# Kernel optimization log

Hardware: AMD Instinct MI355X
Metric: run time of the kernel (lower is better)

## Reference

```python
import jax, jax.numpy as jnp
import numpy as np

B, T, D, W, H = 8, 2048, 1024, 16, 8
HD = D // H  # head dim = 128
EPS = 1e-5


def _layernorm(x, g, b):
    m = jnp.mean(x, axis=-1, keepdims=True)
    v = jnp.var(x, axis=-1, keepdims=True)
    return (x - m) / jnp.sqrt(v + EPS) * g + b


def setup_inputs() -> dict:
    key = jax.random.key(0)
    ks = jax.random.split(key, 8)
    s = 0.02
    return {
        "frame_features": jax.random.normal(ks[0], (B, T, D), dtype=jnp.float32),
        "frame_indices": jnp.arange(B * T, dtype=jnp.int64).reshape(B, T),
        # nn.MultiheadAttention packed in-projection (3D, D) and out projection
        "w_qkv": jax.random.normal(ks[1], (3 * D, D), dtype=jnp.float32) * s,
        "b_qkv": jnp.zeros((3 * D,), dtype=jnp.float32),
        "w_out": jax.random.normal(ks[2], (D, D), dtype=jnp.float32) * s,
        "b_out": jnp.zeros((D,), dtype=jnp.float32),
        # FFN: Linear(D, 4D) -> GELU -> Linear(4D, D)
        "w1": jax.random.normal(ks[3], (4 * D, D), dtype=jnp.float32) * s,
        "b1": jnp.zeros((4 * D,), dtype=jnp.float32),
        "w2": jax.random.normal(ks[4], (D, 4 * D), dtype=jnp.float32) * s,
        "b2": jnp.zeros((D,), dtype=jnp.float32),
        "g1": jnp.ones((D,), dtype=jnp.float32),
        "beta1": jnp.zeros((D,), dtype=jnp.float32),
        "g2": jnp.ones((D,), dtype=jnp.float32),
        "beta2": jnp.zeros((D,), dtype=jnp.float32),
    }


def _forward(frame_features, frame_indices, w_qkv, b_qkv, w_out, b_out,
             w1, b1, w2, b2, g1, beta1, g2, beta2):
    # --- sinusoidal temporal positional encoding, indexed by frame number ---
    pos = frame_indices.astype(jnp.float32)[..., None]          # (B, T, 1)
    div = jnp.exp(-jnp.log(10000.0) * jnp.arange(0, D, 2, dtype=jnp.float32) / D)
    ang = pos * div                                              # (B, T, D/2)
    pe = jnp.stack([jnp.sin(ang), jnp.cos(ang)], axis=-1).reshape(B, T, D)
    x = frame_features + pe

    # --- block-diagonal (local window) attention, all windows in one pass ---
    nw = T // W
    xw = x.reshape(B, nw, W, D)
    qkv = jnp.einsum('bnwd,ed->bnwe', xw, w_qkv) + b_qkv         # (B, nw, W, 3D)
    q, k, v = jnp.split(qkv, 3, axis=-1)
    q = q.reshape(B, nw, W, H, HD)
    k = k.reshape(B, nw, W, H, HD)
    v = v.reshape(B, nw, W, H, HD)
    scores = jnp.einsum('bnqhd,bnkhd->bnhqk', q, k) / jnp.sqrt(jnp.float32(HD))
    attn = jax.nn.softmax(scores, axis=-1)
    o = jnp.einsum('bnhqk,bnkhd->bnqhd', attn, v).reshape(B, nw, W, D)
    attn_out = jnp.einsum('bnwd,ed->bnwe', o, w_out) + b_out

    h = _layernorm(xw + attn_out, g1, beta1)
    ffn = jnp.einsum('bnwf,df->bnwd', jax.nn.gelu(
        jnp.einsum('bnwd,fd->bnwf', h, w1) + b1, approximate=False), w2) + b2
    out = _layernorm(h + ffn, g2, beta2)
    return out.reshape(B, T, D)


def reference(frame_features, frame_indices, w_qkv, b_qkv, w_out, b_out,
              w1, b1, w2, b2, g1, beta1, g2, beta2):
    return _forward(frame_features, frame_indices, w_qkv, b_qkv, w_out, b_out,
                    w1, b1, w2, b2, g1, beta1, g2, beta2)
```

## Files before the change

kernel.cpp:

```cpp
#include <hip/hip_runtime.h>
#include <math.h>

typedef __bf16 bf16;
typedef __bf16 bf16x8 __attribute__((ext_vector_type(8)));
typedef __bf16 bf16x4 __attribute__((ext_vector_type(4)));
typedef __bf16 bf16x2 __attribute__((ext_vector_type(2)));
typedef float f32x4 __attribute__((ext_vector_type(4)));

#define ROWS 16384

typedef __attribute__((address_space(3))) void* lds_vp;
typedef const __attribute__((address_space(1))) void* glb_vp;
__device__ __forceinline__ void gload16(const void* g, void* l) {
  __builtin_amdgcn_global_load_lds((glb_vp)g, (lds_vp)l, 16, 0, 0);
}

__global__ __launch_bounds__(256) void cast_kernel(
    const float* __restrict__ src, bf16* __restrict__ dst, int n)
{
  int i = (blockIdx.x * 256 + threadIdx.x) * 8;
  if (i >= n) return;
  float4 a = *(const float4*)(src + i);
  float4 b = *(const float4*)(src + i + 4);
  bf16x8 o;
  o[0] = (bf16)a.x; o[1] = (bf16)a.y; o[2] = (bf16)a.z; o[3] = (bf16)a.w;
  o[4] = (bf16)b.x; o[5] = (bf16)b.y; o[6] = (bf16)b.z; o[7] = (bf16)b.w;
  *(bf16x8*)(dst + i) = o;
}

__global__ __launch_bounds__(256) void pe_add_kernel(
    const float* __restrict__ ff, const int* __restrict__ idx, bf16* __restrict__ x)
{
  int p   = blockIdx.x * 256 + threadIdx.x;
  int row = p >> 9;
  int j   = p & 511;
  float pos = (float)idx[row];
  float d2  = (float)(2 * j) * (1.0f / 1024.0f);
  float dv  = expf(-9.210340371976184f * d2);
  float ang = pos * dv;
  float s, c;
  sincosf(ang, &s, &c);
  int base = row * 1024 + 2 * j;
  float2 f = *(const float2*)(ff + base);
  bf16x2 o;
  o[0] = (bf16)(f.x + s);
  o[1] = (bf16)(f.y + c);
  *(bf16x2*)(x + base) = o;
}

#define MFMA16 __builtin_amdgcn_mfma_f32_16x16x32_bf16
#define SB  __builtin_amdgcn_sched_barrier(0)
#define BAR asm volatile("s_barrier" ::: "memory")

template<bool GELU, bool RES>
__global__ __launch_bounds__(512, 2) void gemm8(
    const bf16* __restrict__ A, const bf16* __restrict__ Bw,
    const float* __restrict__ bias, const bf16* __restrict__ resid,
    bf16* __restrict__ C, int M, int N, int K)
{
  extern __shared__ char smem[];
  bf16* lA = (bf16*)smem;
  bf16* lB = (bf16*)(smem + 65536);

  const int tid  = threadIdx.x;
  const int wave = tid >> 6;
  const int lane = tid & 63;
  const int wm = wave >> 2, wn = wave & 3;
  const int ln = lane & 15, q = lane >> 4;
  const int wm8 = wm * 8, wn4 = wn * 4;
  const int rsw = (ln * 32 + q * 8) ^ (((ln >> 3) & 1) << 4);

  const int nwg = gridDim.x;
  const int nbm = M >> 8;
  const int swz = (blockIdx.x & 7) * (nwg >> 3) + (blockIdx.x >> 3);
  const int bm = (swz % nbm) << 8;
  const int bn = (swz / nbm) << 8;

  const int le = lane ^ (((lane >> 5) & 1) << 1);
  const int sr = le >> 2;
  const int sc = (le & 3) * 8;
  const bf16* gA = A  + (size_t)(bm + wave * 16 + sr) * K + sc;
  const bf16* gB = Bw + (size_t)(bn + wave * 16 + sr) * K + sc;
  const size_t hstep = (size_t)128 * K;

#define STAGE_A(h, bb, kk) do { \
    bf16* _d = lA + (bb) * 16384 + ((h) * 8 + wave) * 1024; \
    gload16(gA + (size_t)(h) * hstep + (kk), _d); \
    gload16(gA + (size_t)(h) * hstep + (kk) + 32, _d + 512); } while (0)
#define STAGE_B(h, bb, kk) do { \
    bf16* _d = lB + (bb) * 16384 + ((h) * 8 + wave) * 1024; \
    gload16(gB + (size_t)(h) * hstep + (kk), _d); \
    gload16(gB + (size_t)(h) * hstep + (kk) + 32, _d + 512); } while (0)
#define LDA8(dst, t, ks, bb) (dst) = *(const bf16x8*)(lA + (bb) * 16384 + (wm8 + (t)) * 1024 + (ks) * 512 + rsw)
#define LDB8(dst, n, ks, bb) (dst) = *(const bf16x8*)(lB + (bb) * 16384 + (wn4 + (n)) * 1024 + (ks) * 512 + rsw)

  f32x4 acc[8][4];
#pragma unroll
  for (int i = 0; i < 8; i++)
#pragma unroll
    for (int j = 0; j < 4; j++) acc[i][j] = {0.f, 0.f, 0.f, 0.f};

  const int nkt = K >> 6;

  STAGE_A(0, 0, 0);  STAGE_A(1, 0, 0);
  STAGE_B(0, 0, 0);  STAGE_B(1, 0, 0);
  STAGE_A(0, 1, 64); STAGE_A(1, 1, 64);
  SB; asm volatile("s_waitcnt vmcnt(4)" ::: "memory"); SB;
  BAR; SB;

  bf16x8 alo[4][2], ahi[4][2], bq[2][2];

  for (int m = 0; m < nkt; ++m) {
    const int b  = m & 1;
    const int k0 = m << 6;

#pragma unroll
    for (int t = 0; t < 4; t++) { LDA8(alo[t][0], t, 0, b); LDA8(alo[t][1], t, 1, b); }
    LDB8(bq[0][0], 0, 0, b); LDB8(bq[0][1], 0, 1, b);
    LDB8(bq[1][0], 1, 0, b); LDB8(bq[1][1], 1, 1, b);
    if (m + 1 < nkt) STAGE_B(0, b ^ 1, k0 + 64);
    SB; BAR; SB;
    __builtin_amdgcn_s_setprio(1);
#pragma unroll
    for (int t = 0; t < 4; t++)
#pragma unroll
      for (int n = 0; n < 2; n++) {
        acc[t][n] = MFMA16(alo[t][0], bq[n][0], acc[t][n], 0, 0, 0);
        acc[t][n] = MFMA16(alo[t][1], bq[n][1], acc[t][n], 0, 0, 0);
      }
    __builtin_amdgcn_s_setprio(0);
    SB; BAR; SB;

#pragma unroll
    for (int t = 0; t < 4; t++) { LDA8(ahi[t][0], t + 4, 0, b); LDA8(ahi[t][1], t + 4, 1, b); }
    if (m + 1 < nkt) STAGE_B(1, b ^ 1, k0 + 64);
    SB; BAR; SB;
    __builtin_amdgcn_s_setprio(1);
#pragma unroll
    for (int t = 0; t < 4; t++)
#pragma unroll
      for (int n = 0; n < 2; n++) {
        acc[t + 4][n] = MFMA16(ahi[t][0], bq[n][0], acc[t + 4][n], 0, 0, 0);
        acc[t + 4][n] = MFMA16(ahi[t][1], bq[n][1], acc[t + 4][n], 0, 0, 0);
      }
    __builtin_amdgcn_s_setprio(0);
    SB; BAR; SB;

    LDB8(bq[0][0], 2, 0, b); LDB8(bq[0][1], 2, 1, b);
    LDB8(bq[1][0], 3, 0, b); LDB8(bq[1][1], 3, 1, b);
    if (m + 2 < nkt) STAGE_A(0, b, k0 + 128);
    SB; BAR; SB;
    __builtin_amdgcn_s_setprio(1);
#pragma unroll
    for (int t = 0; t < 4; t++)
#pragma unroll
      for (int n = 0; n < 2; n++) {
        acc[t][n + 2] = MFMA16(alo[t][0], bq[n][0], acc[t][n + 2], 0, 0, 0);
        acc[t][n + 2] = MFMA16(alo[t][1], bq[n][1], acc[t][n + 2], 0, 0, 0);
      }
    __builtin_amdgcn_s_setprio(0);
    SB; BAR; SB;

    if (m + 2 < nkt) STAGE_A(1, b, k0 + 128);
    SB; BAR; SB;
    __builtin_amdgcn_s_setprio(1);
#pragma unroll
    for (int t = 0; t < 4; t++)
#pragma unroll
      for (int n = 0; n < 2; n++) {
        acc[t + 4][n + 2] = MFMA16(ahi[t][0], bq[n][0], acc[t + 4][n + 2], 0, 0, 0);
        acc[t + 4][n + 2] = MFMA16(ahi[t][1], bq[n][1], acc[t + 4][n + 2], 0, 0, 0);
      }
    __builtin_amdgcn_s_setprio(0);
    SB;
    if (m == nkt - 2)     { asm volatile("s_waitcnt vmcnt(0)" ::: "memory"); }
    else if (m < nkt - 2) { asm volatile("s_waitcnt vmcnt(4)" ::: "memory"); }
    SB; BAR; SB;
  }

  float bv[4];
#pragma unroll
  for (int tn = 0; tn < 4; tn++) bv[tn] = bias[bn + wn * 64 + tn * 16 + ln];
  bf16* eb = (bf16*)smem;
  const int lrow = tid >> 4;
  const int cb   = (tid & 15) * 16;
#pragma unroll
  for (int tm = 0; tm < 8; tm++) {
    __syncthreads();
#pragma unroll
    for (int tn = 0; tn < 4; tn++)
#pragma unroll
      for (int i = 0; i < 4; i++)
        eb[(wm * 16 + q * 4 + i) * 264 + wn * 64 + tn * 16 + ln] =
            (bf16)(acc[tm][tn][i] + bv[tn]);
    __syncthreads();
    int gR = bm + (lrow >> 4) * 128 + tm * 16 + (lrow & 15);
    size_t rowoff = (size_t)gR * N + bn + cb;
    bf16x8 v0 = *(const bf16x8*)&eb[lrow * 264 + cb];
    bf16x8 v1 = *(const bf16x8*)&eb[lrow * 264 + cb + 8];
    if (RES) {
      bf16x8 r0 = *(const bf16x8*)(resid + rowoff);
      bf16x8 r1 = *(const bf16x8*)(resid + rowoff + 8);
#pragma unroll
      for (int u = 0; u < 8; u++) {
        v0[u] = (bf16)((float)v0[u] + (float)r0[u]);
        v1[u] = (bf16)((float)v1[u] + (float)r1[u]);
      }
    }
    if (GELU) {
#pragma unroll
      for (int u = 0; u < 8; u++) {
        float a = (float)v0[u], c = (float)v1[u];
        v0[u] = (bf16)(0.5f * a * (1.0f + erff(a * 0.70710678118654752f)));
        v1[u] = (bf16)(0.5f * c * (1.0f + erff(c * 0.70710678118654752f)));
      }
    }
    *(bf16x8*)(C + rowoff)     = v0;
    *(bf16x8*)(C + rowoff + 8) = v1;
  }
#undef STAGE_A
#undef STAGE_B
#undef LDA8
#undef LDB8
}

__global__ __launch_bounds__(256) void attn_kernel(
    const bf16* __restrict__ qkv, bf16* __restrict__ o)
{
  __shared__ float sq[16][132], sk[16][132], sv[16][132];
  __shared__ float ss[16][17];

  int wid = blockIdx.x;
  int h   = wid & 7;
  int win = wid >> 3;
  int tb  = win * 16;

  int t  = threadIdx.x;
  int r  = t >> 4;
  int c8 = (t & 15) * 8;

  const bf16* base = qkv + (size_t)(tb + r) * 3072 + c8;
  bf16x8 qv = *(const bf16x8*)(base + h * 128);
  bf16x8 kv = *(const bf16x8*)(base + 1024 + h * 128);
  bf16x8 vv = *(const bf16x8*)(base + 2048 + h * 128);
#pragma unroll
  for (int u = 0; u < 8; u++) {
    sq[r][c8 + u] = (float)qv[u];
    sk[r][c8 + u] = (float)kv[u];
    sv[r][c8 + u] = (float)vv[u];
  }
  __syncthreads();

  {
    int i = t >> 4, jj = t & 15;
    float s = 0.f;
#pragma unroll 8
    for (int d = 0; d < 128; d++) s += sq[i][d] * sk[jj][d];
    ss[i][jj] = s * 0.08838834764831845f;
  }
  __syncthreads();

  if (t < 16) {
    float m = -1e30f;
    for (int jj = 0; jj < 16; jj++) m = fmaxf(m, ss[t][jj]);
    float sum = 0.f;
    for (int jj = 0; jj < 16; jj++) { float e = expf(ss[t][jj] - m); ss[t][jj] = e; sum += e; }
    float inv = 1.0f / sum;
    for (int jj = 0; jj < 16; jj++) ss[t][jj] *= inv;
  }
  __syncthreads();

  {
    int i = t >> 4; int d0 = (t & 15) * 8;
    float acc[8] = {0, 0, 0, 0, 0, 0, 0, 0};
#pragma unroll
    for (int jj = 0; jj < 16; jj++) {
      float a = ss[i][jj];
#pragma unroll
      for (int u = 0; u < 8; u++) acc[u] += a * sv[jj][d0 + u];
    }
    bf16* op = o + (size_t)(tb + i) * 1024 + h * 128 + d0;
#pragma unroll
    for (int u = 0; u < 8; u++) op[u] = (bf16)acc[u];
  }
}

template<typename OUT_T>
__global__ __launch_bounds__(256) void ln_kernel(
    const bf16* __restrict__ x, const float* __restrict__ g,
    const float* __restrict__ b, OUT_T* __restrict__ y)
{
  __shared__ float red[8];
  int row = blockIdx.x;
  int t   = threadIdx.x;
  int lane = t & 63, wave = t >> 6;

  bf16x4 v4 = *(const bf16x4*)(x + (size_t)row * 1024 + t * 4);
  float v[4];
  float s = 0.f, sq = 0.f;
#pragma unroll
  for (int u = 0; u < 4; u++) {
    v[u] = (float)v4[u];
    s += v[u];
    sq += v[u] * v[u];
  }
  for (int off = 32; off > 0; off >>= 1) {
    s  += __shfl_down(s, off);
    sq += __shfl_down(sq, off);
  }
  if (lane == 0) { red[wave * 2] = s; red[wave * 2 + 1] = sq; }
  __syncthreads();
  float st = red[0] + red[2] + red[4] + red[6];
  float qt = red[1] + red[3] + red[5] + red[7];
  float mean = st * (1.0f / 1024.0f);
  float var  = qt * (1.0f / 1024.0f) - mean * mean;
  float inv  = rsqrtf(var + 1e-5f);
  int c = t * 4;
  OUT_T* yr = y + (size_t)row * 1024 + c;
#pragma unroll
  for (int u = 0; u < 4; u++)
    yr[u] = (OUT_T)((v[u] - mean) * inv * g[c + u] + b[c + u]);
}

extern "C" void kernel_launch(void* const* d_in, const int* in_sizes, int n_in,
                              void* d_out, int out_size, void* d_ws, size_t ws_size,
                              hipStream_t stream) {
  const float* ff    = (const float*)d_in[0];
  const int*   idx   = (const int*)d_in[1];
  const float* w_qkv = (const float*)d_in[2];
  const float* b_qkv = (const float*)d_in[3];
  const float* w_out = (const float*)d_in[4];
  const float* b_out = (const float*)d_in[5];
  const float* w1    = (const float*)d_in[6];
  const float* b1    = (const float*)d_in[7];
  const float* w2    = (const float*)d_in[8];
  const float* b2    = (const float*)d_in[9];
  const float* g1    = (const float*)d_in[10];
  const float* be1   = (const float*)d_in[11];
  const float* g2    = (const float*)d_in[12];
  const float* be2   = (const float*)d_in[13];
  float* out = (float*)d_out;

  static bool attrs_done = false;
  if (!attrs_done) {
    attrs_done = true;
    hipFuncSetAttribute(reinterpret_cast<const void*>(&gemm8<false, false>),
                        hipFuncAttributeMaxDynamicSharedMemorySize, 131072);
    hipFuncSetAttribute(reinterpret_cast<const void*>(&gemm8<false, true>),
                        hipFuncAttributeMaxDynamicSharedMemorySize, 131072);
    hipFuncSetAttribute(reinterpret_cast<const void*>(&gemm8<true, false>),
                        hipFuncAttributeMaxDynamicSharedMemorySize, 131072);
  }

  char* p = (char*)d_ws;
  bf16* x_bf = (bf16*)p;  p += (size_t)ROWS * 1024 * 2;
  bf16* big  = (bf16*)p;  p += (size_t)ROWS * 4096 * 2;
  bf16* s_bf = (bf16*)p;  p += (size_t)ROWS * 1024 * 2;
  bf16* h_bf = (bf16*)p;  p += (size_t)ROWS * 1024 * 2;
  bf16* wqb  = (bf16*)p;  p += (size_t)3072 * 1024 * 2;
  bf16* wob  = (bf16*)p;  p += (size_t)1024 * 1024 * 2;
  bf16* w1b  = (bf16*)p;  p += (size_t)4096 * 1024 * 2;
  bf16* w2b  = (bf16*)p;  p += (size_t)1024 * 4096 * 2;
  bf16* o_bf = big + (size_t)ROWS * 3072;
  bf16* g_bf = big;

  cast_kernel<<<3072 * 1024 / 8 / 256, 256, 0, stream>>>(w_qkv, wqb, 3072 * 1024);
  cast_kernel<<<1024 * 1024 / 8 / 256, 256, 0, stream>>>(w_out, wob, 1024 * 1024);
  cast_kernel<<<4096 * 1024 / 8 / 256, 256, 0, stream>>>(w1, w1b, 4096 * 1024);
  cast_kernel<<<1024 * 4096 / 8 / 256, 256, 0, stream>>>(w2, w2b, 1024 * 4096);

  pe_add_kernel<<<ROWS * 512 / 256, 256, 0, stream>>>(ff, idx, x_bf);

  gemm8<false, false><<<64 * 12, 512, 131072, stream>>>(
      x_bf, wqb, b_qkv, nullptr, big, ROWS, 3072, 1024);
  attn_kernel<<<(ROWS / 16) * 8, 256, 0, stream>>>(big, o_bf);
  gemm8<false, true><<<64 * 4, 512, 131072, stream>>>(
      o_bf, wob, b_out, x_bf, s_bf, ROWS, 1024, 1024);
  ln_kernel<bf16><<<ROWS, 256, 0, stream>>>(s_bf, g1, be1, h_bf);
  gemm8<true, false><<<64 * 16, 512, 131072, stream>>>(
      h_bf, w1b, b1, nullptr, big, ROWS, 4096, 1024);
  gemm8<false, true><<<64 * 4, 512, 131072, stream>>>(
      g_bf, w2b, b2, h_bf, s_bf, ROWS, 1024, 4096);
  ln_kernel<float><<<ROWS, 256, 0, stream>>>(s_bf, g2, be2, out);
}
```

Before: 727.2 us.

## Reorder GEMM tile mapping, relax barrier memory clobbers, use tanh-approx GELU

Changes the workgroup-to-tile mapping so consecutive swizzled blocks walk along N instead of M. Replaces inline-asm barriers that had memory clobbers with the builtin s_barrier and adds explicit lgkmcnt waits, giving the compiler more freedom to schedule. Replaces the erf-based GELU in the epilogue with a tanh approximation built from exp2 and rcp. This makes GELU cheaper but departs from the exact erf GELU the reference specifies.

```diff
diff --git a/kernel.cpp b/kernel.cpp
--- a/kernel.cpp
+++ b/kernel.cpp
@@ -50,7 +50,6 @@
 
 #define MFMA16 __builtin_amdgcn_mfma_f32_16x16x32_bf16
 #define SB  __builtin_amdgcn_sched_barrier(0)
-#define BAR asm volatile("s_barrier" ::: "memory")
 
 template<bool GELU, bool RES>
 __global__ __launch_bounds__(512, 2) void gemm8(
@@ -71,10 +70,10 @@
   const int rsw = (ln * 32 + q * 8) ^ (((ln >> 3) & 1) << 4);
 
   const int nwg = gridDim.x;
-  const int nbm = M >> 8;
+  const int nbn = N >> 8;
   const int swz = (blockIdx.x & 7) * (nwg >> 3) + (blockIdx.x >> 3);
-  const int bm = (swz % nbm) << 8;
-  const int bn = (swz / nbm) << 8;
+  const int bm = (swz / nbn) << 8;
+  const int bn = (swz % nbn) << 8;
 
   const int le = lane ^ (((lane >> 5) & 1) << 1);
   const int sr = le >> 2;
@@ -105,8 +104,8 @@
   STAGE_A(0, 0, 0);  STAGE_A(1, 0, 0);
   STAGE_B(0, 0, 0);  STAGE_B(1, 0, 0);
   STAGE_A(0, 1, 64); STAGE_A(1, 1, 64);
-  SB; asm volatile("s_waitcnt vmcnt(4)" ::: "memory"); SB;
-  BAR; SB;
+  SB; asm volatile("s_waitcnt vmcnt(4)"); SB;
+  __builtin_amdgcn_s_barrier();
 
   bf16x8 alo[4][2], ahi[4][2], bq[2][2];
 
@@ -119,7 +118,9 @@
     LDB8(bq[0][0], 0, 0, b); LDB8(bq[0][1], 0, 1, b);
     LDB8(bq[1][0], 1, 0, b); LDB8(bq[1][1], 1, 1, b);
     if (m + 1 < nkt) STAGE_B(0, b ^ 1, k0 + 64);
-    SB; BAR; SB;
+    __builtin_amdgcn_s_barrier();
+    asm volatile("s_waitcnt lgkmcnt(0)");
+    SB;
     __builtin_amdgcn_s_setprio(1);
 #pragma unroll
     for (int t = 0; t < 4; t++)
@@ -129,12 +130,14 @@
         acc[t][n] = MFMA16(alo[t][1], bq[n][1], acc[t][n], 0, 0, 0);
       }
     __builtin_amdgcn_s_setprio(0);
-    SB; BAR; SB;
+    __builtin_amdgcn_s_barrier();
 
 #pragma unroll
     for (int t = 0; t < 4; t++) { LDA8(ahi[t][0], t + 4, 0, b); LDA8(ahi[t][1], t + 4, 1, b); }
     if (m + 1 < nkt) STAGE_B(1, b ^ 1, k0 + 64);
-    SB; BAR; SB;
+    __builtin_amdgcn_s_barrier();
+    asm volatile("s_waitcnt lgkmcnt(0)");
+    SB;
     __builtin_amdgcn_s_setprio(1);
 #pragma unroll
     for (int t = 0; t < 4; t++)
@@ -144,12 +147,14 @@
         acc[t + 4][n] = MFMA16(ahi[t][1], bq[n][1], acc[t + 4][n], 0, 0, 0);
       }
     __builtin_amdgcn_s_setprio(0);
-    SB; BAR; SB;
+    __builtin_amdgcn_s_barrier();
 
     LDB8(bq[0][0], 2, 0, b); LDB8(bq[0][1], 2, 1, b);
     LDB8(bq[1][0], 3, 0, b); LDB8(bq[1][1], 3, 1, b);
     if (m + 2 < nkt) STAGE_A(0, b, k0 + 128);
-    SB; BAR; SB;
+    __builtin_amdgcn_s_barrier();
+    asm volatile("s_waitcnt lgkmcnt(0)");
+    SB;
     __builtin_amdgcn_s_setprio(1);
 #pragma unroll
     for (int t = 0; t < 4; t++)
@@ -159,10 +164,10 @@
         acc[t][n + 2] = MFMA16(alo[t][1], bq[n][1], acc[t][n + 2], 0, 0, 0);
       }
     __builtin_amdgcn_s_setprio(0);
-    SB; BAR; SB;
+    __builtin_amdgcn_s_barrier();
 
     if (m + 2 < nkt) STAGE_A(1, b, k0 + 128);
-    SB; BAR; SB;
+    __builtin_amdgcn_s_barrier();
     __builtin_amdgcn_s_setprio(1);
 #pragma unroll
     for (int t = 0; t < 4; t++)
@@ -173,9 +178,10 @@
       }
     __builtin_amdgcn_s_setprio(0);
     SB;
-    if (m == nkt - 2)     { asm volatile("s_waitcnt vmcnt(0)" ::: "memory"); }
-    else if (m < nkt - 2) { asm volatile("s_waitcnt vmcnt(4)" ::: "memory"); }
-    SB; BAR; SB;
+    if (m == nkt - 2)     { asm volatile("s_waitcnt vmcnt(0)"); }
+    else if (m < nkt - 2) { asm volatile("s_waitcnt vmcnt(4)"); }
+    SB;
+    __builtin_amdgcn_s_barrier();
   }
 
   float bv[4];
@@ -211,8 +217,10 @@
 #pragma unroll
       for (int u = 0; u < 8; u++) {
         float a = (float)v0[u], c = (float)v1[u];
-        v0[u] = (bf16)(0.5f * a * (1.0f + erff(a * 0.70710678118654752f)));
-        v1[u] = (bf16)(0.5f * c * (1.0f + erff(c * 0.70710678118654752f)));
+        float ea = __builtin_amdgcn_exp2f(2.3022082f * a * (1.0f + 0.044715f * a * a));
+        float ec = __builtin_amdgcn_exp2f(2.3022082f * c * (1.0f + 0.044715f * c * c));
+        v0[u] = (bf16)(a - a * __builtin_amdgcn_rcpf(ea + 1.0f));
+        v1[u] = (bf16)(c - c * __builtin_amdgcn_rcpf(ec + 1.0f));
       }
     }
     *(bf16x8*)(C + rowoff)     = v0;
```

Result: faster. 671.1 us (-7.7%).
